# Kernel optimization log

Measured on AMD Instinct MI355X. Metric: run time of the kernel, lower is better.

## Reference

```python
import jax, jax.numpy as jnp
import numpy as np

B, N, D = 16, 2048, 128
NEG = jnp.float32(-2.0**32 + 1)

def setup_inputs() -> dict:
    key = jax.random.key(0)
    ks = jax.random.split(key, 9)
    s = 1.0 / np.sqrt(D)
    return {
        "queries": jax.random.normal(ks[0], (B, N, D), jnp.float32),
        "keys": jax.random.normal(ks[1], (B, N, D), jnp.float32),
        "padding_mask": jax.random.randint(ks[2], (B, N), 0, 2, jnp.int32),
        "Wq": jax.random.uniform(ks[3], (D, D), jnp.float32, -s, s),
        "bq": jax.random.uniform(ks[4], (D,), jnp.float32, -s, s),
        "Wk": jax.random.uniform(ks[5], (D, D), jnp.float32, -s, s),
        "bk": jax.random.uniform(ks[6], (D,), jnp.float32, -s, s),
        "Wv": jax.random.uniform(ks[7], (D, D), jnp.float32, -s, s),
        "bv": jax.random.uniform(ks[8], (D,), jnp.float32, -s, s),
    }

def reference(queries, keys, padding_mask, Wq, bq, Wk, bk, Wv, bv):
    d = queries.shape[-1]
    eq = queries @ Wq.T + bq            # [B,N,D]
    ek = keys @ Wk.T + bk               # [B,N,D]
    ev = keys @ Wv.T + bv               # [B,N,D]
    # scaled scores [B,N,N]
    coefs = jnp.einsum('bnd,bmd->bnm', eq, ek) / jnp.sqrt(jnp.float32(d))
    # key padding: large negative where keys row sums to zero (broadcast over query axis)
    key_pad = (jnp.sum(keys, axis=-1) == 0).astype(jnp.float32) * NEG   # [B,N]
    out = jnp.where(padding_mask[:, None, :] == 0, key_pad[:, None, :], coefs)
    out = jax.nn.softmax(out, axis=2)
    # NOTE: original applies query mask along the KEY axis (unsqueeze(1)) -- kept faithfully
    q_pad = (jnp.sum(queries, axis=-1) != 0).astype(jnp.float32)        # [B,N]
    out = out * q_pad[:, None, :]
    out = jnp.einsum('bnm,bmd->bnd', out, ev)
    return out + queries
```

## Files before the change

### kernel.cpp

```cpp
#include <hip/hip_runtime.h>
#include <hip/hip_bf16.h>


#define SCALE_LOG2E 0.12751875f

typedef __bf16 bf16x8 __attribute__((ext_vector_type(8)));
typedef float  f32x4  __attribute__((ext_vector_type(4)));

static __device__ __forceinline__ float fexp2(float x) {
#if __has_builtin(__builtin_amdgcn_exp2f)
    return __builtin_amdgcn_exp2f(x);
#else
    float r; asm("v_exp_f32 %0, %1" : "=v"(r) : "v"(x)); return r;
#endif
}

static __device__ __forceinline__ void gl16(const __bf16* g, __bf16* l) {
    __builtin_amdgcn_global_load_lds(
        (const __attribute__((address_space(1))) unsigned int*)g,
        (__attribute__((address_space(3))) unsigned int*)l, 16, 0, 0);
}

__global__ __launch_bounds__(256) void prep_kernel(
    const float* __restrict__ Wq, const float* __restrict__ Wk,
    const float* __restrict__ Wv, __bf16* __restrict__ wb)
{
    int i = blockIdx.x * 256 + threadIdx.x;
    int w = i >> 11, c = i & 2047;
    int col = c & 15, quad = (c >> 4) & 3, f = (c >> 6) & 3, ct = c >> 8;
    const float* src = ((w == 0) ? Wq : (w == 1) ? Wk : Wv)
                       + (size_t)(ct * 16 + col) * 128 + f * 32 + quad * 8;
    float4 a = *(const float4*)src, b = *(const float4*)(src + 4);
    bf16x8 t = {(__bf16)a.x, (__bf16)a.y, (__bf16)a.z, (__bf16)a.w,
                (__bf16)b.x, (__bf16)b.y, (__bf16)b.z, (__bf16)b.w};
    *(bf16x8*)&wb[(size_t)w * 16384 + (size_t)c * 8] = t;
}

__global__ __launch_bounds__(256) void proj_kernel(
    const float* __restrict__ Q, const float* __restrict__ K,
    const int* __restrict__ PM, const __bf16* __restrict__ wb,
    const float* __restrict__ Bq, const float* __restrict__ Bk,
    const float* __restrict__ Bv,
    __bf16* __restrict__ eqb, __bf16* __restrict__ ekf, __bf16* __restrict__ evf,
    float* __restrict__ madd)
{
    __shared__ __bf16 stage[128 * 72];
    const int tid  = threadIdx.x;
    const int wave = tid >> 6, lane = tid & 63;
    const int col  = lane & 15, quad = lane >> 4;
    const int w = blockIdx.x >> 9;
    const int rowbase = (blockIdx.x & 511) * 64;
    const int myrow   = rowbase + wave * 16 + col;
    const int bb   = rowbase >> 11;
    const int m16b = (rowbase & 2047) >> 4;

    const float* asrc = (w == 0) ? Q : K;
    bf16x8 a[4];
    float ss = 0.f;
    #pragma unroll
    for (int f = 0; f < 4; ++f) {
        const float* p = asrc + (size_t)myrow * 128 + f * 32 + quad * 8;
        float4 v0 = *(const float4*)p, v1 = *(const float4*)(p + 4);
        float vv[8] = {v0.x, v0.y, v0.z, v0.w, v1.x, v1.y, v1.z, v1.w};
        #pragma unroll
        for (int j = 0; j < 8; ++j) { ss += vv[j]; a[f][j] = (__bf16)vv[j]; }
    }

    float rm = 1.f;
    if (w == 1) {
        ss += __shfl_xor(ss, 16); ss += __shfl_xor(ss, 32);
        int pmv = PM[myrow];
        rm = (pmv != 0) ? 1.f : 0.f;
        if (quad == 0) madd[myrow] = (pmv == 0 && ss == 0.f) ? -1.0e5f : 0.f;
    } else if (w == 2) {
        float qs = 0.f;
        #pragma unroll
        for (int f = 0; f < 4; ++f) {
            const float* p = Q + (size_t)myrow * 128 + f * 32 + quad * 8;
            float4 v0 = *(const float4*)p, v1 = *(const float4*)(p + 4);
            qs += v0.x + v0.y + v0.z + v0.w + v1.x + v1.y + v1.z + v1.w;
        }
        qs += __shfl_xor(qs, 16); qs += __shfl_xor(qs, 32);
        rm = (qs != 0.f) ? 1.f : 0.f;
    }
    float rmul[4];
    #pragma unroll
    for (int r = 0; r < 4; ++r) rmul[r] = __shfl(rm, quad * 4 + r);

    const float sc = (w == 0) ? SCALE_LOG2E : 1.f;
    const float* bias = (w == 0) ? Bq : (w == 1) ? Bk : Bv;
    const __bf16* wbp = wb + w * 16384;

    f32x4 acc[8];
    #pragma unroll
    for (int ct = 0; ct < 8; ++ct) { f32x4 z = {0.f, 0.f, 0.f, 0.f}; acc[ct] = z; }
    #pragma unroll
    for (int f = 0; f < 4; ++f) {
        #pragma unroll
        for (int ct = 0; ct < 8; ++ct) {
            bf16x8 bfr = *(const bf16x8*)&wbp[(size_t)(ct * 4 + f) * 512 + lane * 8];
            acc[ct] = __builtin_amdgcn_mfma_f32_16x16x32_bf16(a[f], bfr, acc[ct], 0, 0, 0);
        }
    }
    #pragma unroll
    for (int ct = 0; ct < 8; ++ct) {
        float bv = bias[ct * 16 + col];
        #pragma unroll
        for (int r = 0; r < 4; ++r) {
            float v = (acc[ct][r] + bv) * rmul[r] * sc;
            int rr = wave * 16 + quad * 4 + r;
            if (w == 2) stage[(ct * 16 + col) * 72 + rr] = (__bf16)v;
            else        stage[rr * 136 + ct * 16 + col] = (__bf16)v;
        }
    }
    __syncthreads();

    if (w == 0) {
        int r = tid >> 2, seg = (tid & 3) * 32;
        uint4* g4 = (uint4*)(eqb + (size_t)(rowbase + r) * 128 + seg);
        const uint4* s4 = (const uint4*)&stage[r * 136 + seg];
        g4[0] = s4[0]; g4[1] = s4[1]; g4[2] = s4[2]; g4[3] = s4[3];
    } else if (w == 1) {
        __bf16* dst = ekf + (size_t)bb * 2048 * 128 + (size_t)m16b * 2048;
        #pragma unroll
        for (int c = 0; c < 4; ++c) {
            int s = tid + c * 256;
            int l = s & 63, f = (s >> 6) & 3, m = s >> 8;
            *(uint4*)&dst[(size_t)s * 8] =
                *(const uint4*)&stage[(m * 16 + (l & 15)) * 136 + f * 32 + ((l >> 4) & 3) * 8];
        }
    } else {
        __bf16* dst = evf + (size_t)bb * 2048 * 128 + (size_t)(rowbase & 2047) * 128;
        #pragma unroll
        for (int c = 0; c < 4; ++c) {
            int s = tid + c * 256;
            int l = s & 63, dt = (s >> 6) & 7, tl = s >> 9;
            int cl = l & 15, ql = l >> 4;
            uint2 xa = *(const uint2*)&stage[(dt * 16 + cl) * 72 + tl * 32 + ql * 4];
            uint2 xb = *(const uint2*)&stage[(dt * 16 + cl) * 72 + tl * 32 + 16 + ql * 4];
            uint4 v = {xa.x, xa.y, xb.x, xb.y};
            *(uint4*)&dst[(size_t)s * 8] = v;
        }
    }
}

__global__ __launch_bounds__(256, 2) void attn_kernel(
    const __bf16* __restrict__ eqb, const __bf16* __restrict__ ekf,
    const __bf16* __restrict__ evf, const float* __restrict__ madd,
    const float* __restrict__ Q, float* __restrict__ out)
{
    __shared__ union {
        __bf16 vstage[4][4096];
        struct { float obuf[32 * 132]; float lbuf[2][32]; } cmb;
    } sm;

    const int tid  = threadIdx.x;
    const int wave = tid >> 6, lane = tid & 63;
    const int col  = lane & 15, quad = lane >> 4;
    const int i  = blockIdx.x;
    const int b  = 2 * (i & 7) + ((i >> 3) & 1);
    const int qt = i >> 4;
    const int rowg0 = b * 2048 + qt * 32;
    const __bf16* ekb_b = ekf + (size_t)b * 2048 * 128;
    const __bf16* evb_b = evf + (size_t)b * 2048 * 128;
    const float*  dmb   = madd + b * 2048;

    bf16x8 aqf[2][4];
    #pragma unroll
    for (int q2 = 0; q2 < 2; ++q2)
        #pragma unroll
        for (int f = 0; f < 4; ++f)
            aqf[q2][f] = *(const bf16x8*)&eqb[(size_t)(rowg0 + q2 * 16 + col) * 128 + f * 32 + quad * 8];

    f32x4 o[2][8];
    float lsum[2] = {0.f, 0.f};
    #pragma unroll
    for (int q2 = 0; q2 < 2; ++q2)
        #pragma unroll
        for (int dt = 0; dt < 8; ++dt) { f32x4 z = {0.f, 0.f, 0.f, 0.f}; o[q2][dt] = z; }

    const int kq0 = wave * 512;

    {
        const int t32 = kq0 >> 5;
        #pragma unroll
        for (int dt = 0; dt < 8; ++dt)
            gl16(evb_b + (size_t)(t32 * 8 + dt) * 512 + lane * 8,
                 &sm.vstage[wave][dt * 512]);
    }
    bf16x8 kc[8];
    {
        const int m16 = kq0 >> 4;
        #pragma unroll
        for (int f = 0; f < 4; ++f) {
            kc[f]     = *(const bf16x8*)&ekb_b[(size_t)((m16 + 0) * 4 + f) * 512 + lane * 8];
            kc[4 + f] = *(const bf16x8*)&ekb_b[(size_t)((m16 + 1) * 4 + f) * 512 + lane * 8];
        }
    }
    float4 dm0 = *(const float4*)&dmb[kq0 + quad * 4];
    float4 dm1 = *(const float4*)&dmb[kq0 + 16 + quad * 4];

    for (int it = 0; it < 16; ++it) {
        const int kb = kq0 + it * 32;

        bf16x8 kn[8];
        float4 dn0, dn1;
        if (it < 15) {
            const int m16n = (kb >> 4) + 2;
            #pragma unroll
            for (int f = 0; f < 4; ++f) {
                kn[f]     = *(const bf16x8*)&ekb_b[(size_t)((m16n + 0) * 4 + f) * 512 + lane * 8];
                kn[4 + f] = *(const bf16x8*)&ekb_b[(size_t)((m16n + 1) * 4 + f) * 512 + lane * 8];
            }
            dn0 = *(const float4*)&dmb[kb + 32 + quad * 4];
            dn1 = *(const float4*)&dmb[kb + 48 + quad * 4];
        }
        __builtin_amdgcn_sched_barrier(0);

        f32x4 s[2][2];
        {
            f32x4 i0 = {dm0.x, dm0.y, dm0.z, dm0.w};
            f32x4 i1 = {dm1.x, dm1.y, dm1.z, dm1.w};
            s[0][0] = i0; s[0][1] = i1; s[1][0] = i0; s[1][1] = i1;
        }
        __builtin_amdgcn_s_setprio(1);
        #pragma unroll
        for (int f = 0; f < 4; ++f) {
            #pragma unroll
            for (int q2 = 0; q2 < 2; ++q2) {
                s[q2][0] = __builtin_amdgcn_mfma_f32_16x16x32_bf16(kc[f],     aqf[q2][f], s[q2][0], 0, 0, 0);
                s[q2][1] = __builtin_amdgcn_mfma_f32_16x16x32_bf16(kc[4 + f], aqf[q2][f], s[q2][1], 0, 0, 0);
            }
        }
        __builtin_amdgcn_s_setprio(0);

        bf16x8 pq[2];
        #pragma unroll
        for (int q2 = 0; q2 < 2; ++q2)
            #pragma unroll
            for (int g = 0; g < 2; ++g)
                #pragma unroll
                for (int r = 0; r < 4; ++r) {
                    float e = fexp2(s[q2][g][r]);
                    pq[q2][g * 4 + r] = (__bf16)e;
                    lsum[q2] += e;
                }

        if (it < 15) asm volatile("s_waitcnt vmcnt(10)" ::: "memory");
        else         asm volatile("s_waitcnt vmcnt(0)"  ::: "memory");
        __builtin_amdgcn_sched_barrier(0);

        bf16x8 vf[8];
        #pragma unroll
        for (int dt = 0; dt < 8; ++dt)
            vf[dt] = *(const bf16x8*)&sm.vstage[wave][dt * 512 + lane * 8];
        asm volatile("s_waitcnt lgkmcnt(0)" ::: "memory");
        __builtin_amdgcn_sched_barrier(0);

        if (it < 15) {
            const int t32n = (kb >> 5) + 1;
            #pragma unroll
            for (int dt = 0; dt < 8; ++dt)
                gl16(evb_b + (size_t)(t32n * 8 + dt) * 512 + lane * 8,
                     &sm.vstage[wave][dt * 512]);
        }

        __builtin_amdgcn_s_setprio(1);
        #pragma unroll
        for (int dt = 0; dt < 8; ++dt) {
            #pragma unroll
            for (int q2 = 0; q2 < 2; ++q2)
                o[q2][dt] = __builtin_amdgcn_mfma_f32_16x16x32_bf16(vf[dt], pq[q2], o[q2][dt], 0, 0, 0);
        }
        __builtin_amdgcn_s_setprio(0);

        if (it < 15) {
            #pragma unroll
            for (int f = 0; f < 8; ++f) kc[f] = kn[f];
            dm0 = dn0; dm1 = dn1;
        }
    }

    #pragma unroll
    for (int q2 = 0; q2 < 2; ++q2) {
        lsum[q2] += __shfl_xor(lsum[q2], 16);
        lsum[q2] += __shfl_xor(lsum[q2], 32);
    }

    __syncthreads();

    if (wave == 1) {
        #pragma unroll
        for (int q2 = 0; q2 < 2; ++q2) {
            #pragma unroll
            for (int dt = 0; dt < 8; ++dt) {
                float4 v = {o[q2][dt][0], o[q2][dt][1], o[q2][dt][2], o[q2][dt][3]};
                *(float4*)&sm.cmb.obuf[(q2 * 16 + col) * 132 + dt * 16 + quad * 4] = v;
            }
            if (quad == 0) sm.cmb.lbuf[0][q2 * 16 + col] = lsum[q2];
        }
    }
    __syncthreads();
    if (wave == 0) {
        #pragma unroll
        for (int q2 = 0; q2 < 2; ++q2) {
            lsum[q2] += sm.cmb.lbuf[0][q2 * 16 + col];
            #pragma unroll
            for (int dt = 0; dt < 8; ++dt) {
                float4 t = *(const float4*)&sm.cmb.obuf[(q2 * 16 + col) * 132 + dt * 16 + quad * 4];
                o[q2][dt][0] += t.x; o[q2][dt][1] += t.y;
                o[q2][dt][2] += t.z; o[q2][dt][3] += t.w;
            }
        }
    }
    __syncthreads();
    if (wave == 3) {
        #pragma unroll
        for (int q2 = 0; q2 < 2; ++q2) {
            #pragma unroll
            for (int dt = 0; dt < 8; ++dt) {
                float4 v = {o[q2][dt][0], o[q2][dt][1], o[q2][dt][2], o[q2][dt][3]};
                *(float4*)&sm.cmb.obuf[(q2 * 16 + col) * 132 + dt * 16 + quad * 4] = v;
            }
            if (quad == 0) sm.cmb.lbuf[1][q2 * 16 + col] = lsum[q2];
        }
    }
    __syncthreads();
    if (wave == 2) {
        #pragma unroll
        for (int q2 = 0; q2 < 2; ++q2) {
            lsum[q2] += sm.cmb.lbuf[1][q2 * 16 + col];
            #pragma unroll
            for (int dt = 0; dt < 8; ++dt) {
                float4 t = *(const float4*)&sm.cmb.obuf[(q2 * 16 + col) * 132 + dt * 16 + quad * 4];
                float4 v = {o[q2][dt][0] + t.x, o[q2][dt][1] + t.y,
                            o[q2][dt][2] + t.z, o[q2][dt][3] + t.w};
                *(float4*)&sm.cmb.obuf[(q2 * 16 + col) * 132 + dt * 16 + quad * 4] = v;
            }
            if (quad == 0) sm.cmb.lbuf[0][q2 * 16 + col] = lsum[q2];
        }
    }
    __syncthreads();
    if (wave == 0) {
        #pragma unroll
        for (int q2 = 0; q2 < 2; ++q2) {
            float inv = 1.f / (lsum[q2] + sm.cmb.lbuf[0][q2 * 16 + col]);
            const size_t rowoff = (size_t)(rowg0 + q2 * 16 + col) * 128;
            #pragma unroll
            for (int dt = 0; dt < 8; ++dt) {
                float4 t = *(const float4*)&sm.cmb.obuf[(q2 * 16 + col) * 132 + dt * 16 + quad * 4];
                f32x4 qres = __builtin_nontemporal_load((const f32x4*)&Q[rowoff + dt * 16 + quad * 4]);
                f32x4 v;
                v[0] = (o[q2][dt][0] + t.x) * inv + qres[0];
                v[1] = (o[q2][dt][1] + t.y) * inv + qres[1];
                v[2] = (o[q2][dt][2] + t.z) * inv + qres[2];
                v[3] = (o[q2][dt][3] + t.w) * inv + qres[3];
                __builtin_nontemporal_store(v, (f32x4*)&out[rowoff + dt * 16 + quad * 4]);
            }
        }
    }
}

extern "C" void kernel_launch(void* const* d_in, const int* in_sizes, int n_in,
                              void* d_out, int out_size, void* d_ws, size_t ws_size,
                              hipStream_t stream)
{
    const float* Q  = (const float*)d_in[0];
    const float* K  = (const float*)d_in[1];
    const int*   PM = (const int*)d_in[2];
    const float* Wq = (const float*)d_in[3];
    const float* Bq = (const float*)d_in[4];
    const float* Wk = (const float*)d_in[5];
    const float* Bk = (const float*)d_in[6];
    const float* Wv = (const float*)d_in[7];
    const float* Bv = (const float*)d_in[8];
    float* out = (float*)d_out;

    const size_t SZE = (size_t)16 * 2048 * 128;
    __bf16* eqb = (__bf16*)d_ws;
    __bf16* ekf = eqb + SZE;
    __bf16* evf = ekf + SZE;
    float* madd = (float*)(evf + SZE);
    __bf16* wb  = (__bf16*)(madd + 16 * 2048);

    prep_kernel<<<24, 256, 0, stream>>>(Wq, Wk, Wv, wb);
    proj_kernel<<<1536, 256, 0, stream>>>(Q, K, PM, wb, Bq, Bk, Bv,
                                          eqb, ekf, evf, madd);
    attn_kernel<<<1024, 256, 0, stream>>>(eqb, ekf, evf, madd, Q, out);
}
```

Measured before the change: 161.5 us.

## Double query rows per attention block, stage Q in LDS, drop K/V prefetch

Each attention block now handles 64 query rows instead of 32, and the grid is halved, so every K/V tile loaded from global memory serves twice as many queries. Query fragments are staged once in LDS and re-read with inline ds_read_b128 per 16-row group, which saves registers that the larger output accumulator now needs. The software prefetch of K/mask into registers and the async global-to-LDS V staging are removed in favour of direct loads each iteration. This exposes memory latency and leaves only 512 blocks, which may underfill the GPU and lower occupancy.

```diff
diff --git a/kernel.cpp b/kernel.cpp
--- a/kernel.cpp
+++ b/kernel.cpp
@@ -6,6 +6,7 @@
 
 typedef __bf16 bf16x8 __attribute__((ext_vector_type(8)));
 typedef float  f32x4  __attribute__((ext_vector_type(4)));
+typedef int    i32x4  __attribute__((ext_vector_type(4)));
 
 static __device__ __forceinline__ float fexp2(float x) {
 #if __has_builtin(__builtin_amdgcn_exp2f)
@@ -13,12 +14,6 @@
 #else
     float r; asm("v_exp_f32 %0, %1" : "=v"(r) : "v"(x)); return r;
 #endif
-}
-
-static __device__ __forceinline__ void gl16(const __bf16* g, __bf16* l) {
-    __builtin_amdgcn_global_load_lds(
-        (const __attribute__((address_space(1))) unsigned int*)g,
-        (__attribute__((address_space(3))) unsigned int*)l, 16, 0, 0);
 }
 
 __global__ __launch_bounds__(256) void prep_kernel(
@@ -150,8 +145,8 @@
     const float* __restrict__ Q, float* __restrict__ out)
 {
     __shared__ union {
-        __bf16 vstage[4][4096];
-        struct { float obuf[32 * 132]; float lbuf[2][32]; } cmb;
+        __bf16 qlds[8192];
+        struct { float obuf[64 * 132]; float lbuf[2][64]; } cmb;
     } sm;
 
     const int tid  = threadIdx.x;
@@ -160,129 +155,101 @@
     const int i  = blockIdx.x;
     const int b  = 2 * (i & 7) + ((i >> 3) & 1);
     const int qt = i >> 4;
-    const int rowg0 = b * 2048 + qt * 32;
+    const int rowg0 = b * 2048 + qt * 64;
     const __bf16* ekb_b = ekf + (size_t)b * 2048 * 128;
     const __bf16* evb_b = evf + (size_t)b * 2048 * 128;
     const float*  dmb   = madd + b * 2048;
 
-    bf16x8 aqf[2][4];
-    #pragma unroll
-    for (int q2 = 0; q2 < 2; ++q2)
-        #pragma unroll
-        for (int f = 0; f < 4; ++f)
-            aqf[q2][f] = *(const bf16x8*)&eqb[(size_t)(rowg0 + q2 * 16 + col) * 128 + f * 32 + quad * 8];
-
-    f32x4 o[2][8];
-    float lsum[2] = {0.f, 0.f};
-    #pragma unroll
-    for (int q2 = 0; q2 < 2; ++q2)
+    #pragma unroll
+    for (int c = 0; c < 4; ++c) {
+        int s = tid + c * 256;
+        int l = s & 63, f = (s >> 6) & 3, q2 = s >> 8;
+        *(uint4*)&sm.qlds[(size_t)s * 8] =
+            *(const uint4*)&eqb[(size_t)(rowg0 + q2 * 16 + (l & 15)) * 128 + f * 32 + ((l >> 4) & 3) * 8];
+    }
+    __syncthreads();
+    const unsigned qaddr =
+        (unsigned)(uintptr_t)(__attribute__((address_space(3))) __bf16*)&sm.qlds[0]
+        + (unsigned)lane * 16u;
+
+    f32x4 o[4][8];
+    float lsum[4] = {0.f, 0.f, 0.f, 0.f};
+    #pragma unroll
+    for (int q2 = 0; q2 < 4; ++q2)
         #pragma unroll
         for (int dt = 0; dt < 8; ++dt) { f32x4 z = {0.f, 0.f, 0.f, 0.f}; o[q2][dt] = z; }
 
     const int kq0 = wave * 512;
 
-    {
-        const int t32 = kq0 >> 5;
-        #pragma unroll
-        for (int dt = 0; dt < 8; ++dt)
-            gl16(evb_b + (size_t)(t32 * 8 + dt) * 512 + lane * 8,
-                 &sm.vstage[wave][dt * 512]);
-    }
-    bf16x8 kc[8];
-    {
-        const int m16 = kq0 >> 4;
+    for (int it = 0; it < 16; ++it) {
+        const int kb  = kq0 + it * 32;
+        const int m16 = kb >> 4, t32 = kb >> 5;
+
+        bf16x8 kc[8], vf[8];
         #pragma unroll
         for (int f = 0; f < 4; ++f) {
             kc[f]     = *(const bf16x8*)&ekb_b[(size_t)((m16 + 0) * 4 + f) * 512 + lane * 8];
             kc[4 + f] = *(const bf16x8*)&ekb_b[(size_t)((m16 + 1) * 4 + f) * 512 + lane * 8];
         }
-    }
-    float4 dm0 = *(const float4*)&dmb[kq0 + quad * 4];
-    float4 dm1 = *(const float4*)&dmb[kq0 + 16 + quad * 4];
-
-    for (int it = 0; it < 16; ++it) {
-        const int kb = kq0 + it * 32;
-
-        bf16x8 kn[8];
-        float4 dn0, dn1;
-        if (it < 15) {
-            const int m16n = (kb >> 4) + 2;
-            #pragma unroll
-            for (int f = 0; f < 4; ++f) {
-                kn[f]     = *(const bf16x8*)&ekb_b[(size_t)((m16n + 0) * 4 + f) * 512 + lane * 8];
-                kn[4 + f] = *(const bf16x8*)&ekb_b[(size_t)((m16n + 1) * 4 + f) * 512 + lane * 8];
-            }
-            dn0 = *(const float4*)&dmb[kb + 32 + quad * 4];
-            dn1 = *(const float4*)&dmb[kb + 48 + quad * 4];
-        }
-        __builtin_amdgcn_sched_barrier(0);
-
-        f32x4 s[2][2];
-        {
-            f32x4 i0 = {dm0.x, dm0.y, dm0.z, dm0.w};
-            f32x4 i1 = {dm1.x, dm1.y, dm1.z, dm1.w};
-            s[0][0] = i0; s[0][1] = i1; s[1][0] = i0; s[1][1] = i1;
-        }
+        #pragma unroll
+        for (int dt = 0; dt < 8; ++dt)
+            vf[dt] = *(const bf16x8*)&evb_b[((size_t)t32 * 8 + dt) * 512 + lane * 8];
+        float4 dm0 = *(const float4*)&dmb[kb + quad * 4];
+        float4 dm1 = *(const float4*)&dmb[kb + 16 + quad * 4];
+
+        bf16x8 pq[4];
+        #pragma unroll
+        for (int q2 = 0; q2 < 4; ++q2) {
+            unsigned qa = qaddr + (unsigned)q2 * 4096u;
+            i32x4 a0, a1, a2, a3;
+            asm volatile(
+                "ds_read_b128 %0, %4 offset:0\n\t"
+                "ds_read_b128 %1, %4 offset:1024\n\t"
+                "ds_read_b128 %2, %4 offset:2048\n\t"
+                "ds_read_b128 %3, %4 offset:3072\n\t"
+                "s_waitcnt lgkmcnt(0)"
+                : "=&v"(a0), "=&v"(a1), "=&v"(a2), "=&v"(a3)
+                : "v"(qa));
+            __builtin_amdgcn_sched_barrier(0);
+            bf16x8 aq0, aq1, aq2, aq3;
+            __builtin_memcpy(&aq0, &a0, 16); __builtin_memcpy(&aq1, &a1, 16);
+            __builtin_memcpy(&aq2, &a2, 16); __builtin_memcpy(&aq3, &a3, 16);
+
+            f32x4 s0 = {dm0.x, dm0.y, dm0.z, dm0.w};
+            f32x4 s1 = {dm1.x, dm1.y, dm1.z, dm1.w};
+            __builtin_amdgcn_s_setprio(1);
+            s0 = __builtin_amdgcn_mfma_f32_16x16x32_bf16(kc[0], aq0, s0, 0, 0, 0);
+            s1 = __builtin_amdgcn_mfma_f32_16x16x32_bf16(kc[4], aq0, s1, 0, 0, 0);
+            s0 = __builtin_amdgcn_mfma_f32_16x16x32_bf16(kc[1], aq1, s0, 0, 0, 0);
+            s1 = __builtin_amdgcn_mfma_f32_16x16x32_bf16(kc[5], aq1, s1, 0, 0, 0);
+            s0 = __builtin_amdgcn_mfma_f32_16x16x32_bf16(kc[2], aq2, s0, 0, 0, 0);
+            s1 = __builtin_amdgcn_mfma_f32_16x16x32_bf16(kc[6], aq2, s1, 0, 0, 0);
+            s0 = __builtin_amdgcn_mfma_f32_16x16x32_bf16(kc[3], aq3, s0, 0, 0, 0);
+            s1 = __builtin_amdgcn_mfma_f32_16x16x32_bf16(kc[7], aq3, s1, 0, 0, 0);
+            __builtin_amdgcn_s_setprio(0);
+
+            #pragma unroll
+            for (int r = 0; r < 4; ++r) {
+                float e0 = fexp2(s0[r]);
+                float e1 = fexp2(s1[r]);
+                pq[q2][r]     = (__bf16)e0;
+                pq[q2][4 + r] = (__bf16)e1;
+                lsum[q2] += e0 + e1;
+            }
+        }
+
         __builtin_amdgcn_s_setprio(1);
         #pragma unroll
-        for (int f = 0; f < 4; ++f) {
-            #pragma unroll
-            for (int q2 = 0; q2 < 2; ++q2) {
-                s[q2][0] = __builtin_amdgcn_mfma_f32_16x16x32_bf16(kc[f],     aqf[q2][f], s[q2][0], 0, 0, 0);
-                s[q2][1] = __builtin_amdgcn_mfma_f32_16x16x32_bf16(kc[4 + f], aqf[q2][f], s[q2][1], 0, 0, 0);
-            }
+        for (int dt = 0; dt < 8; ++dt) {
+            #pragma unroll
+            for (int q2 = 0; q2 < 4; ++q2)
+                o[q2][dt] = __builtin_amdgcn_mfma_f32_16x16x32_bf16(vf[dt], pq[q2], o[q2][dt], 0, 0, 0);
         }
         __builtin_amdgcn_s_setprio(0);
-
-        bf16x8 pq[2];
-        #pragma unroll
-        for (int q2 = 0; q2 < 2; ++q2)
-            #pragma unroll
-            for (int g = 0; g < 2; ++g)
-                #pragma unroll
-                for (int r = 0; r < 4; ++r) {
-                    float e = fexp2(s[q2][g][r]);
-                    pq[q2][g * 4 + r] = (__bf16)e;
-                    lsum[q2] += e;
-                }
-
-        if (it < 15) asm volatile("s_waitcnt vmcnt(10)" ::: "memory");
-        else         asm volatile("s_waitcnt vmcnt(0)"  ::: "memory");
-        __builtin_amdgcn_sched_barrier(0);
-
-        bf16x8 vf[8];
-        #pragma unroll
-        for (int dt = 0; dt < 8; ++dt)
-            vf[dt] = *(const bf16x8*)&sm.vstage[wave][dt * 512 + lane * 8];
-        asm volatile("s_waitcnt lgkmcnt(0)" ::: "memory");
-        __builtin_amdgcn_sched_barrier(0);
-
-        if (it < 15) {
-            const int t32n = (kb >> 5) + 1;
-            #pragma unroll
-            for (int dt = 0; dt < 8; ++dt)
-                gl16(evb_b + (size_t)(t32n * 8 + dt) * 512 + lane * 8,
-                     &sm.vstage[wave][dt * 512]);
-        }
-
-        __builtin_amdgcn_s_setprio(1);
-        #pragma unroll
-        for (int dt = 0; dt < 8; ++dt) {
-            #pragma unroll
-            for (int q2 = 0; q2 < 2; ++q2)
-                o[q2][dt] = __builtin_amdgcn_mfma_f32_16x16x32_bf16(vf[dt], pq[q2], o[q2][dt], 0, 0, 0);
-        }
-        __builtin_amdgcn_s_setprio(0);
-
-        if (it < 15) {
-            #pragma unroll
-            for (int f = 0; f < 8; ++f) kc[f] = kn[f];
-            dm0 = dn0; dm1 = dn1;
-        }
-    }
-
-    #pragma unroll
-    for (int q2 = 0; q2 < 2; ++q2) {
+    }
+
+    #pragma unroll
+    for (int q2 = 0; q2 < 4; ++q2) {
         lsum[q2] += __shfl_xor(lsum[q2], 16);
         lsum[q2] += __shfl_xor(lsum[q2], 32);
     }
@@ -291,7 +258,7 @@
 
     if (wave == 1) {
         #pragma unroll
-        for (int q2 = 0; q2 < 2; ++q2) {
+        for (int q2 = 0; q2 < 4; ++q2) {
             #pragma unroll
             for (int dt = 0; dt < 8; ++dt) {
                 float4 v = {o[q2][dt][0], o[q2][dt][1], o[q2][dt][2], o[q2][dt][3]};
@@ -303,7 +270,7 @@
     __syncthreads();
     if (wave == 0) {
         #pragma unroll
-        for (int q2 = 0; q2 < 2; ++q2) {
+        for (int q2 = 0; q2 < 4; ++q2) {
             lsum[q2] += sm.cmb.lbuf[0][q2 * 16 + col];
             #pragma unroll
             for (int dt = 0; dt < 8; ++dt) {
@@ -316,7 +283,7 @@
     __syncthreads();
     if (wave == 3) {
         #pragma unroll
-        for (int q2 = 0; q2 < 2; ++q2) {
+        for (int q2 = 0; q2 < 4; ++q2) {
             #pragma unroll
             for (int dt = 0; dt < 8; ++dt) {
                 float4 v = {o[q2][dt][0], o[q2][dt][1], o[q2][dt][2], o[q2][dt][3]};
@@ -328,7 +295,7 @@
     __syncthreads();
     if (wave == 2) {
         #pragma unroll
-        for (int q2 = 0; q2 < 2; ++q2) {
+        for (int q2 = 0; q2 < 4; ++q2) {
             lsum[q2] += sm.cmb.lbuf[1][q2 * 16 + col];
             #pragma unroll
             for (int dt = 0; dt < 8; ++dt) {
@@ -343,7 +310,7 @@
     __syncthreads();
     if (wave == 0) {
         #pragma unroll
-        for (int q2 = 0; q2 < 2; ++q2) {
+        for (int q2 = 0; q2 < 4; ++q2) {
             float inv = 1.f / (lsum[q2] + sm.cmb.lbuf[0][q2 * 16 + col]);
             const size_t rowoff = (size_t)(rowg0 + q2 * 16 + col) * 128;
             #pragma unroll
@@ -386,5 +353,5 @@
     prep_kernel<<<24, 256, 0, stream>>>(Wq, Wk, Wv, wb);
     proj_kernel<<<1536, 256, 0, stream>>>(Q, K, PM, wb, Bq, Bk, Bv,
                                           eqb, ekf, evf, madd);
-    attn_kernel<<<1024, 256, 0, stream>>>(eqb, ekf, evf, madd, Q, out);
-}
+    attn_kernel<<<512, 256, 0, stream>>>(eqb, ekf, evf, madd, Q, out);
+}
```

Result: faster. 152.9 us (-5.3%).
